# Kernel tuning notes

Hardware: AMD Instinct MI355X
Metric: run time of the kernel (lower is better)

The kernel has to match this reference:

```python
import jax, jax.numpy as jnp
import numpy as np

B, T, D_MODEL, H, D = 2, 2048, 2048, 16, 128


def _rope_tables(t, d_half, base=10000.0):
    inv_freq = 1.0 / (base ** (jnp.arange(d_half, dtype=jnp.float32) / d_half))
    ang = jnp.arange(t, dtype=jnp.float32)[:, None] * inv_freq[None, :]  # (T, D/2)
    return jnp.cos(ang), jnp.sin(ang)


def setup_inputs() -> dict:
    key = jax.random.key(0)
    ks = jax.random.split(key, 5)
    x = jax.random.normal(ks[0], (B, T, D_MODEL), dtype=jnp.float32)
    mask = jnp.tril(jnp.ones((T, T), dtype=bool))  # causal boolean mask
    cos, sin = _rope_tables(T, D // 2)
    std = 1.0 / np.sqrt(D_MODEL)
    Wq = jax.random.normal(ks[1], (D_MODEL, H * D), dtype=jnp.float32) * std
    Wk = jax.random.normal(ks[2], (D_MODEL, H * D), dtype=jnp.float32) * std
    Wv = jax.random.normal(ks[3], (D_MODEL, H * D), dtype=jnp.float32) * std
    Wo = jax.random.normal(ks[4], (H * D, D_MODEL), dtype=jnp.float32) * std
    return {"x": x, "mask": mask, "cos": cos, "sin": sin,
            "Wq": Wq, "Wk": Wk, "Wv": Wv, "Wo": Wo}


def _apply_rope(x, cos, sin):
    # x: (B, H, T, D); cos/sin: (T, D/2)
    half = x.shape[-1] // 2
    x1, x2 = x[..., :half], x[..., half:]
    c = cos[None, None]
    s = sin[None, None]
    return jnp.concatenate([x1 * c - x2 * s, x1 * s + x2 * c], axis=-1)


def reference(x, mask, cos, sin, Wq, Wk, Wv, Wo):
    b, t, _ = x.shape
    scale = 1.0 / np.sqrt(D)
    # projections: (B, T, H*D) -> (B, H, T, D)
    q = (x @ Wq).reshape(b, t, H, D).transpose(0, 2, 1, 3)
    k = (x @ Wk).reshape(b, t, H, D).transpose(0, 2, 1, 3)
    v = (x @ Wv).reshape(b, t, H, D).transpose(0, 2, 1, 3)
    q = _apply_rope(q, cos, sin)
    k = _apply_rope(k, cos, sin)
    scores = jnp.einsum('bhqd,bhkd->bhqk', q, k) * scale
    scores = jnp.where(mask[None, None], scores, jnp.float32(-1e30))
    attn = jax.nn.softmax(scores, axis=-1)
    out = jnp.einsum('bhqk,bhkd->bhqd', attn, v)  # (B, H, T, D)
    out = out.transpose(0, 2, 1, 3).reshape(b, t, H * D)
    return out @ Wo
```

## Files before the change

### kernel.cpp

```cpp
#include <hip/hip_runtime.h>

#define T_SEQ 2048
#define DM    2048
#define NH    16
#define HD    128
#define NROW  4096

typedef __attribute__((ext_vector_type(8))) short short8;
typedef __attribute__((ext_vector_type(4))) float f32x4;
typedef __attribute__((ext_vector_type(16))) float f32x16;

static __device__ __forceinline__ float bf2f(unsigned short h) {
    unsigned int u = ((unsigned int)h) << 16;
    return __builtin_bit_cast(float, u);
}
static __device__ __forceinline__ unsigned short f2bf(float f) {
    unsigned int u = __builtin_bit_cast(unsigned int, f);
    u += 0x7FFFu + ((u >> 16) & 1u);
    return (unsigned short)(u >> 16);
}
static __device__ __forceinline__ unsigned short bf_fast(float f) {
    return (unsigned short)((__builtin_bit_cast(unsigned int, f) + 0x8000u) >> 16);
}

typedef __attribute__((address_space(1))) const unsigned int gas_uint;
typedef __attribute__((address_space(3))) unsigned int las_uint;

static __device__ __forceinline__ void load_lds16(const void* g, void* l) {
    __builtin_amdgcn_global_load_lds((gas_uint*)g, (las_uint*)l, 16, 0, 0);
}

static __device__ __forceinline__ f32x4 mfma_bf16(short8 a, short8 b, f32x4 c) {
    return __builtin_amdgcn_mfma_f32_16x16x32_bf16(a, b, c, 0, 0, 0);
}
static __device__ __forceinline__ f32x16 mfma32_bf16(short8 a, short8 b, f32x16 c) {
    return __builtin_amdgcn_mfma_f32_32x32x16_bf16(a, b, c, 0, 0, 0);
}

__global__ __launch_bounds__(256) void k_cast(const float* __restrict__ x,
                                              unsigned short* __restrict__ xb, int n) {
    int idx = (blockIdx.x * 256 + threadIdx.x) * 4;
    if (idx >= n) return;
    float4 v = *(const float4*)(x + idx);
    ushort4 o;
    o.x = f2bf(v.x); o.y = f2bf(v.y); o.z = f2bf(v.z); o.w = f2bf(v.w);
    *(ushort4*)(xb + idx) = o;
}

__global__ __launch_bounds__(256) void k_transpose(const float* __restrict__ w0, const float* __restrict__ w1,
                                                   const float* __restrict__ w2, const float* __restrict__ w3,
                                                   unsigned short* __restrict__ t0, unsigned short* __restrict__ t1,
                                                   unsigned short* __restrict__ t2, unsigned short* __restrict__ t3) {
    __shared__ float tile[32][33];
    int z = blockIdx.z;
    const float* W = (z == 0) ? w0 : (z == 1) ? w1 : (z == 2) ? w2 : w3;
    unsigned short* Wt = (z == 0) ? t0 : (z == 1) ? t1 : (z == 2) ? t2 : t3;
    int bx = blockIdx.x * 32;
    int by = blockIdx.y * 32;
    int tx = threadIdx.x, ty = threadIdx.y;
#pragma unroll
    for (int i = 0; i < 4; ++i)
        tile[ty + i * 8][tx] = W[(size_t)(by + ty + i * 8) * DM + bx + tx];
    __syncthreads();
#pragma unroll
    for (int i = 0; i < 4; ++i)
        Wt[(size_t)(bx + ty + i * 8) * DM + by + tx] = f2bf(tile[tx][ty + i * 8]);
}

template <bool FOUT>
static __device__ __forceinline__ void gemm_body(const unsigned short* __restrict__ A,
                                                 const unsigned short* __restrict__ Bt,
                                                 unsigned short* __restrict__ Cb,
                                                 float* __restrict__ Cf) {
    __shared__ unsigned short As[128 * 64];
    __shared__ unsigned short Bs[128 * 64];
    const int tid = threadIdx.x;
    const int w = tid >> 6, lane = tid & 63;
    const int col = lane & 15, quad = lane >> 4;
    const int wm = w >> 1, wn = w & 1;
    const size_t m0 = (size_t)blockIdx.y * 128;
    const size_t n0 = (size_t)blockIdx.x * 128;

    f32x4 acc[4][4];
#pragma unroll
    for (int i = 0; i < 4; ++i)
#pragma unroll
        for (int j = 0; j < 4; ++j)
            acc[i][j] = (f32x4){0.f, 0.f, 0.f, 0.f};

    const int lrow = lane >> 3;
    const int gcol = ((lane & 7) ^ lrow) * 8;

    for (int k0 = 0; k0 < DM; k0 += 64) {
#pragma unroll
        for (int c = w; c < 16; c += 4) {
            load_lds16(A + (m0 + c * 8 + lrow) * DM + k0 + gcol, &As[c * 512]);
            load_lds16(Bt + (n0 + c * 8 + lrow) * DM + k0 + gcol, &Bs[c * 512]);
        }
        __syncthreads();
#pragma unroll
        for (int ks = 0; ks < 2; ++ks) {
            short8 af[4], bf[4];
            int g = ks * 4 + quad;
#pragma unroll
            for (int mt = 0; mt < 4; ++mt) {
                int r = wm * 64 + mt * 16 + col;
                af[mt] = *(const short8*)&As[r * 64 + ((g ^ (r & 7)) * 8)];
            }
#pragma unroll
            for (int nt = 0; nt < 4; ++nt) {
                int r = wn * 64 + nt * 16 + col;
                bf[nt] = *(const short8*)&Bs[r * 64 + ((g ^ (r & 7)) * 8)];
            }
#pragma unroll
            for (int mt = 0; mt < 4; ++mt)
#pragma unroll
                for (int nt = 0; nt < 4; ++nt)
                    acc[mt][nt] = mfma_bf16(af[mt], bf[nt], acc[mt][nt]);
        }
        __syncthreads();
    }
#pragma unroll
    for (int mt = 0; mt < 4; ++mt)
#pragma unroll
        for (int nt = 0; nt < 4; ++nt)
#pragma unroll
            for (int reg = 0; reg < 4; ++reg) {
                size_t r = m0 + wm * 64 + mt * 16 + quad * 4 + reg;
                size_t c = n0 + wn * 64 + nt * 16 + col;
                if (FOUT) Cf[r * DM + c] = acc[mt][nt][reg];
                else      Cb[r * DM + c] = f2bf(acc[mt][nt][reg]);
            }
}

__global__ __launch_bounds__(256) void k_gemm_qkv(const unsigned short* __restrict__ xb,
                                                  const unsigned short* __restrict__ wtq,
                                                  const unsigned short* __restrict__ wtk,
                                                  const unsigned short* __restrict__ wtv,
                                                  unsigned short* __restrict__ qb,
                                                  unsigned short* __restrict__ kb,
                                                  unsigned short* __restrict__ vb) {
    int z = blockIdx.z;
    const unsigned short* Bt = (z == 0) ? wtq : (z == 1) ? wtk : wtv;
    unsigned short* C = (z == 0) ? qb : (z == 1) ? kb : vb;
    gemm_body<false>(xb, Bt, C, nullptr);
}

__global__ __launch_bounds__(256) void k_gemm_out(const unsigned short* __restrict__ ob,
                                                  const unsigned short* __restrict__ wto,
                                                  float* __restrict__ out) {
    gemm_body<true>(ob, wto, nullptr, out);
}

__global__ __launch_bounds__(256) void k_rope_k(unsigned short* __restrict__ K,
                                                const float* __restrict__ cosp,
                                                const float* __restrict__ sinp) {
    int idx = blockIdx.x * 256 + threadIdx.x;
    int d4 = (idx & 15) * 4;
    int h = (idx >> 4) & 15;
    int row = idx >> 8;
    int t = row & (T_SEQ - 1);
    size_t base = (size_t)row * DM + h * HD + d4;
    ushort4 x1 = *(const ushort4*)(K + base);
    ushort4 x2 = *(const ushort4*)(K + base + 64);
    float4 c = *(const float4*)(cosp + t * 64 + d4);
    float4 s = *(const float4*)(sinp + t * 64 + d4);
    ushort4 o1, o2;
#pragma unroll
    for (int i = 0; i < 4; ++i) {
        float a1 = bf2f(((const unsigned short*)&x1)[i]);
        float a2 = bf2f(((const unsigned short*)&x2)[i]);
        float cc = ((const float*)&c)[i], ss = ((const float*)&s)[i];
        ((unsigned short*)&o1)[i] = f2bf(a1 * cc - a2 * ss);
        ((unsigned short*)&o2)[i] = f2bf(a1 * ss + a2 * cc);
    }
    *(ushort4*)(K + base) = o1;
    *(ushort4*)(K + base + 64) = o2;
}

__global__ __launch_bounds__(256) void k_vtr(const unsigned short* __restrict__ V,
                                             unsigned short* __restrict__ Vt) {
    __shared__ unsigned short tile[64][68];
    int t0 = blockIdx.x * 64;
    int hd0 = blockIdx.y * 64;
    int b = blockIdx.z;
    int tid = threadIdx.x;
    int rr = tid >> 4, cc = (tid & 15) * 4;
#pragma unroll
    for (int it = 0; it < 4; ++it) {
        int row = it * 16 + rr;
        *(ushort4*)&tile[row][cc] =
            *(const ushort4*)(V + (size_t)(b * T_SEQ + t0 + row) * DM + hd0 + cc);
    }
    __syncthreads();
    int h = hd0 >> 7, d0 = hd0 & 127;
    size_t obase = (size_t)(b * NH + h) * HD;
#pragma unroll
    for (int it = 0; it < 4; ++it) {
        int lhd = it * 16 + rr;
        ushort4 v;
#pragma unroll
        for (int j = 0; j < 4; ++j) ((unsigned short*)&v)[j] = tile[cc + j][lhd];
        *(ushort4*)(Vt + (obase + d0 + lhd) * (size_t)T_SEQ + t0 + cc) = v;
    }
}

#define PST 72
__global__ __launch_bounds__(256) void k_flash(const unsigned short* __restrict__ Q,
                                               const unsigned short* __restrict__ K,
                                               const unsigned short* __restrict__ Vt,
                                               unsigned short* __restrict__ O,
                                               const float* __restrict__ cosp,
                                               const float* __restrict__ sinp) {
    __shared__ unsigned short Ks[64 * 128];
    __shared__ unsigned short Vs[128 * 64];
    __shared__ unsigned short Ps[4][32 * PST];
    const int tid = threadIdx.x;
    const int w = tid >> 6, lane = tid & 63;
    const int col = lane & 31, l5 = lane >> 5;
    const int flat = blockIdx.x | (blockIdx.y << 4) | (blockIdx.z << 8);
    const int j = 15 - (flat >> 5);
    const int hb = flat & 31;
    const int h = hb & 15, b = hb >> 4;
    const int q0 = j * 128;
    const size_t rowbase = ((size_t)b * T_SEQ) * DM + (size_t)h * HD;
    const size_t hbase = ((size_t)b * NH + h) * HD;
    const float SCL = 0.088388347648318447f * 1.4426950408889634f;
    unsigned short* Pw = &Ps[w][0];

    const int t = q0 + w * 32 + col;
    short8 qf[8];
    {
        const unsigned short* qp = Q + rowbase + (size_t)t * DM + l5 * 8;
#pragma unroll
        for (int st = 0; st < 8; ++st)
            qf[st] = *(const short8*)(qp + st * 16);
        const float* cp = cosp + t * 64 + l5 * 8;
        const float* sp = sinp + t * 64 + l5 * 8;
#pragma unroll
        for (int st = 0; st < 4; ++st) {
            float4 c0 = *(const float4*)(cp + st * 16);
            float4 c1 = *(const float4*)(cp + st * 16 + 4);
            float4 s0v = *(const float4*)(sp + st * 16);
            float4 s1v = *(const float4*)(sp + st * 16 + 4);
#pragma unroll
            for (int jj = 0; jj < 8; ++jj) {
                float cv = ((jj < 4) ? ((const float*)&c0)[jj] : ((const float*)&c1)[jj - 4]) * SCL;
                float sv = ((jj < 4) ? ((const float*)&s0v)[jj] : ((const float*)&s1v)[jj - 4]) * SCL;
                float a1 = bf2f((unsigned short)qf[st][jj]);
                float a2 = bf2f((unsigned short)qf[st + 4][jj]);
                qf[st][jj]     = (short)f2bf(a1 * cv - a2 * sv);
                qf[st + 4][jj] = (short)f2bf(a1 * sv + a2 * cv);
            }
        }
    }

    f32x16 o[4];
#pragma unroll
    for (int i = 0; i < 4; ++i) o[i] = (f32x16)(0.f);
    float m_i = -1e30f, l_i = 0.f;

    const int kt_max = 2 * j + 1;
    const int kt_lim = (q0 + w * 32 + 31) >> 6;
    const int cswz = col & 7;

    for (int kt = 0; kt <= kt_max; ++kt) {
        const int k0 = kt * 64;
        __syncthreads();
#pragma unroll
        for (int c = 0; c < 4; ++c) {
            const int c4 = w * 4 + c;
            const int krow = c4 * 4 + (lane >> 4);
            const int kpos = lane & 15;
            load_lds16(K + rowbase + (size_t)(k0 + krow) * DM + ((kpos ^ (krow & 7)) * 8),
                       &Ks[c4 * 512]);
            const int vrow = c4 * 8 + (lane >> 3);
            const int vpos = lane & 7;
            load_lds16(Vt + (hbase + vrow) * (size_t)T_SEQ + k0 + ((vpos ^ (vrow & 7)) * 8),
                       &Vs[c4 * 512]);
        }
        __syncthreads();
        if (kt > kt_lim) continue;

        f32x16 s0 = (f32x16)(0.f), s1 = (f32x16)(0.f);
#pragma unroll
        for (int st = 0; st < 8; ++st) {
            const int dg = (2 * st + l5) ^ cswz;
            short8 kf0 = *(const short8*)&Ks[col * 128 + dg * 8];
            short8 kf1 = *(const short8*)&Ks[col * 128 + 4096 + dg * 8];
            s0 = mfma32_bf16(kf0, qf[st], s0);
            s1 = mfma32_bf16(kf1, qf[st], s1);
        }

        if (k0 + 63 > q0 + w * 32) {
            const int kb = k0 + 4 * l5;
#pragma unroll
            for (int r = 0; r < 16; ++r) {
                const int key = kb + (r & 3) + 8 * (r >> 2);
                if (key > t) s0[r] = -1e30f;
                if (key + 32 > t) s1[r] = -1e30f;
            }
        }

        float mx = -1e30f;
#pragma unroll
        for (int r = 0; r < 16; ++r) mx = fmaxf(mx, fmaxf(s0[r], s1[r]));
        mx = fmaxf(mx, __shfl_xor(mx, 32));
        const float mnew = fmaxf(m_i, mx);
        const float alpha = __builtin_amdgcn_exp2f(m_i - mnew);
        m_i = mnew;
        float sum = 0.f;
#pragma unroll
        for (int r = 0; r < 16; ++r) {
            float p0 = __builtin_amdgcn_exp2f(s0[r] - mnew);
            float p1 = __builtin_amdgcn_exp2f(s1[r] - mnew);
            s0[r] = p0; s1[r] = p1;
            sum += p0 + p1;
        }
        sum += __shfl_xor(sum, 32);
        l_i = l_i * alpha + sum;
#pragma unroll
        for (int i = 0; i < 4; ++i) o[i] *= alpha;

#pragma unroll
        for (int g = 0; g < 4; ++g) {
            ushort4 a4, b4;
#pragma unroll
            for (int i = 0; i < 4; ++i) {
                ((unsigned short*)&a4)[i] = bf_fast(s0[g * 4 + i]);
                ((unsigned short*)&b4)[i] = bf_fast(s1[g * 4 + i]);
            }
            *(ushort4*)(Pw + col * PST + g * 8 + 4 * l5)      = a4;
            *(ushort4*)(Pw + col * PST + 32 + g * 8 + 4 * l5) = b4;
        }
        short8 pb[4];
#pragma unroll
        for (int st = 0; st < 4; ++st)
            pb[st] = *(const short8*)(Pw + col * PST + st * 16 + l5 * 8);

#pragma unroll
        for (int ms = 0; ms < 4; ++ms) {
            const int drow = (ms * 32 + col) * 64;
#pragma unroll
            for (int st = 0; st < 4; ++st) {
                const int kg = (2 * st + l5) ^ cswz;
                short8 vf = *(const short8*)&Vs[drow + kg * 8];
                o[ms] = mfma32_bf16(vf, pb[st], o[ms]);
            }
        }
    }

    const float inv = __builtin_amdgcn_rcpf(l_i);
    unsigned short* op = O + rowbase + (size_t)t * DM;
#pragma unroll
    for (int ms = 0; ms < 4; ++ms)
#pragma unroll
        for (int g = 0; g < 4; ++g) {
            ushort4 st4;
#pragma unroll
            for (int i = 0; i < 4; ++i)
                ((unsigned short*)&st4)[i] = bf_fast(o[ms][g * 4 + i] * inv);
            *(ushort4*)(op + ms * 32 + g * 8 + 4 * l5) = st4;
        }
}

extern "C" void kernel_launch(void* const* d_in, const int* in_sizes, int n_in,
                              void* d_out, int out_size, void* d_ws, size_t ws_size,
                              hipStream_t stream) {
    const float* x    = (const float*)d_in[0];
    const float* cosp = (const float*)d_in[2];
    const float* sinp = (const float*)d_in[3];
    const float* Wq   = (const float*)d_in[4];
    const float* Wk   = (const float*)d_in[5];
    const float* Wv   = (const float*)d_in[6];
    const float* Wo   = (const float*)d_in[7];
    float* out = (float*)d_out;

    unsigned short* xb  = (unsigned short*)d_ws;
    unsigned short* wtq = xb  + (size_t)NROW * DM;
    unsigned short* wtk = wtq + (size_t)DM * DM;
    unsigned short* wtv = wtk + (size_t)DM * DM;
    unsigned short* wto = wtv + (size_t)DM * DM;
    unsigned short* qb  = wto + (size_t)DM * DM;
    unsigned short* kb  = qb  + (size_t)NROW * DM;
    unsigned short* vb  = kb  + (size_t)NROW * DM;
    unsigned short* ob  = vb  + (size_t)NROW * DM;
    unsigned short* vt  = xb;

    hipLaunchKernelGGL(k_cast, dim3(8192), dim3(256), 0, stream, x, xb, NROW * DM);
    hipLaunchKernelGGL(k_transpose, dim3(64, 64, 4), dim3(32, 8), 0, stream,
                       Wq, Wk, Wv, Wo, wtq, wtk, wtv, wto);
    hipLaunchKernelGGL(k_gemm_qkv, dim3(16, 32, 3), dim3(256), 0, stream,
                       xb, wtq, wtk, wtv, qb, kb, vb);
    hipLaunchKernelGGL(k_rope_k, dim3(4096), dim3(256), 0, stream, kb, cosp, sinp);
    hipLaunchKernelGGL(k_vtr, dim3(32, 32, 2), dim3(256), 0, stream, vb, vt);
    hipLaunchKernelGGL(k_flash, dim3(16, 16, 2), dim3(256), 0, stream,
                       qb, kb, vt, ob, cosp, sinp);
    hipLaunchKernelGGL(k_gemm_out, dim3(16, 32, 1), dim3(256), 0, stream, ob, wto, out);
}
```

Baseline: 392.2 us.

## Restructure flash attention into single-wave blocks handling two query sub-tiles

New measurement: 637.8 us. +62.6%, slower.

```diff
diff --git a/kernel.cpp b/kernel.cpp
--- a/kernel.cpp
+++ b/kernel.cpp
@@ -206,31 +206,31 @@
 }
 
 #define PST 72
-__global__ __launch_bounds__(256) void k_flash(const unsigned short* __restrict__ Q,
-                                               const unsigned short* __restrict__ K,
-                                               const unsigned short* __restrict__ Vt,
-                                               unsigned short* __restrict__ O,
-                                               const float* __restrict__ cosp,
-                                               const float* __restrict__ sinp) {
-    __shared__ unsigned short Ks[64 * 128];
-    __shared__ unsigned short Vs[128 * 64];
-    __shared__ unsigned short Ps[4][32 * PST];
-    const int tid = threadIdx.x;
-    const int w = tid >> 6, lane = tid & 63;
+__global__ __launch_bounds__(64, 2) void k_flash(const unsigned short* __restrict__ Q,
+                                                 const unsigned short* __restrict__ K,
+                                                 const unsigned short* __restrict__ Vt,
+                                                 unsigned short* __restrict__ O,
+                                                 const float* __restrict__ cosp,
+                                                 const float* __restrict__ sinp) {
+    __shared__ unsigned short Ks[32 * 128];
+    __shared__ unsigned short Vs[128 * 32];
+    __shared__ unsigned short Ps[64 * PST];
+    const int lane = threadIdx.x;
     const int col = lane & 31, l5 = lane >> 5;
-    const int flat = blockIdx.x | (blockIdx.y << 4) | (blockIdx.z << 8);
-    const int j = 15 - (flat >> 5);
-    const int hb = flat & 31;
-    const int h = hb & 15, b = hb >> 4;
-    const int q0 = j * 128;
+    const int flat = blockIdx.x;
+    const int j = 31 - (flat >> 5);
+    const int bh = flat & 31;
+    const int h = bh & 15, b = bh >> 4;
+    const int q0 = j * 64;
     const size_t rowbase = ((size_t)b * T_SEQ) * DM + (size_t)h * HD;
     const size_t hbase = ((size_t)b * NH + h) * HD;
     const float SCL = 0.088388347648318447f * 1.4426950408889634f;
-    unsigned short* Pw = &Ps[w][0];
-
-    const int t = q0 + w * 32 + col;
-    short8 qf[8];
-    {
+
+    const int tA = q0 + col;
+    const int tB = q0 + 32 + col;
+
+    short8 qfA[8], qfB[8];
+    auto load_q = [&](int t, short8* qf) {
         const unsigned short* qp = Q + rowbase + (size_t)t * DM + l5 * 8;
 #pragma unroll
         for (int st = 0; st < 8; ++st)
@@ -253,115 +253,119 @@
                 qf[st + 4][jj] = (short)f2bf(a1 * sv + a2 * cv);
             }
         }
+    };
+    load_q(tA, qfA);
+    load_q(tB, qfB);
+
+    f32x16 oA[4], oB[4];
+#pragma unroll
+    for (int i = 0; i < 4; ++i) { oA[i] = (f32x16)(0.f); oB[i] = (f32x16)(0.f); }
+    float mA = -1e30f, lA = 0.f, mB = -1e30f, lB = 0.f;
+
+    const int cs7 = col & 7;
+    const int kt_lim = 2 * j + 1;
+
+    for (int kt = 0; kt <= kt_lim; ++kt) {
+        const int k0 = kt * 32;
+        const bool bothQ = (kt <= 2 * j);
+
+#pragma unroll
+        for (int c = 0; c < 8; ++c) {
+            const int s = c * 64 + lane;
+            const int key = s >> 4, ck = s & 15;
+            load_lds16(K + rowbase + (size_t)(k0 + key) * DM + ((ck ^ (key & 7)) * 8),
+                       &Ks[c * 512]);
+            const int d = s >> 2, kg = s & 3;
+            load_lds16(Vt + (hbase + d) * (size_t)T_SEQ + k0 + ((kg ^ ((d >> 1) & 3)) * 8),
+                       &Vs[c * 512]);
+        }
+        __builtin_amdgcn_s_waitcnt(0);
+
+        f32x16 sA = (f32x16)(0.f), sB = (f32x16)(0.f);
+#pragma unroll
+        for (int st = 0; st < 8; ++st) {
+            short8 kf = *(const short8*)&Ks[col * 128 + (((st * 2 + l5) ^ cs7) * 8)];
+            sB = mfma32_bf16(kf, qfB[st], sB);
+            if (bothQ) sA = mfma32_bf16(kf, qfA[st], sA);
+        }
+
+        if (kt == 2 * j) {
+#pragma unroll
+            for (int r = 0; r < 16; ++r) {
+                const int key = k0 + (r & 3) + 8 * (r >> 2) + 4 * l5;
+                if (key > tA) sA[r] = -1e30f;
+            }
+        } else if (kt == 2 * j + 1) {
+#pragma unroll
+            for (int r = 0; r < 16; ++r) {
+                const int key = k0 + (r & 3) + 8 * (r >> 2) + 4 * l5;
+                if (key > tB) sB[r] = -1e30f;
+            }
+        }
+
+        auto softmax_half = [&](f32x16& s, f32x16* o, float& m_i, float& l_i, int prow) {
+            float mx = -1e30f;
+#pragma unroll
+            for (int r = 0; r < 16; ++r) mx = fmaxf(mx, s[r]);
+            mx = fmaxf(mx, __shfl_xor(mx, 32));
+            const float mnew = fmaxf(m_i, mx);
+            const float alpha = __builtin_amdgcn_exp2f(m_i - mnew);
+            m_i = mnew;
+            float sum = 0.f;
+#pragma unroll
+            for (int g = 0; g < 4; ++g) {
+                ushort4 st4;
+#pragma unroll
+                for (int i = 0; i < 4; ++i) {
+                    float p = __builtin_amdgcn_exp2f(s[g * 4 + i] - mnew);
+                    sum += p;
+                    ((unsigned short*)&st4)[i] = bf_fast(p);
+                }
+                *(ushort4*)(Ps + prow * PST + 4 * l5 + 8 * g) = st4;
+            }
+            sum += __shfl_xor(sum, 32);
+            l_i = l_i * alpha + sum;
+#pragma unroll
+            for (int i = 0; i < 4; ++i) o[i] *= alpha;
+        };
+        softmax_half(sB, oB, mB, lB, 32 + col);
+        if (bothQ) softmax_half(sA, oA, mA, lA, col);
+
+        short8 pbA[2], pbB[2];
+#pragma unroll
+        for (int st = 0; st < 2; ++st) {
+            pbB[st] = *(const short8*)&Ps[(32 + col) * PST + st * 16 + l5 * 8];
+            if (bothQ) pbA[st] = *(const short8*)&Ps[col * PST + st * 16 + l5 * 8];
+        }
+#pragma unroll
+        for (int ms = 0; ms < 4; ++ms) {
+            const int d = ms * 32 + col;
+            const int dswz = (d >> 1) & 3;
+#pragma unroll
+            for (int st = 0; st < 2; ++st) {
+                short8 vf = *(const short8*)&Vs[d * 32 + (((st * 2 + l5) ^ dswz) * 8)];
+                oB[ms] = mfma32_bf16(vf, pbB[st], oB[ms]);
+                if (bothQ) oA[ms] = mfma32_bf16(vf, pbA[st], oA[ms]);
+            }
+        }
     }
 
-    f32x16 o[4];
-#pragma unroll
-    for (int i = 0; i < 4; ++i) o[i] = (f32x16)(0.f);
-    float m_i = -1e30f, l_i = 0.f;
-
-    const int kt_max = 2 * j + 1;
-    const int kt_lim = (q0 + w * 32 + 31) >> 6;
-    const int cswz = col & 7;
-
-    for (int kt = 0; kt <= kt_max; ++kt) {
-        const int k0 = kt * 64;
-        __syncthreads();
-#pragma unroll
-        for (int c = 0; c < 4; ++c) {
-            const int c4 = w * 4 + c;
-            const int krow = c4 * 4 + (lane >> 4);
-            const int kpos = lane & 15;
-            load_lds16(K + rowbase + (size_t)(k0 + krow) * DM + ((kpos ^ (krow & 7)) * 8),
-                       &Ks[c4 * 512]);
-            const int vrow = c4 * 8 + (lane >> 3);
-            const int vpos = lane & 7;
-            load_lds16(Vt + (hbase + vrow) * (size_t)T_SEQ + k0 + ((vpos ^ (vrow & 7)) * 8),
-                       &Vs[c4 * 512]);
-        }
-        __syncthreads();
-        if (kt > kt_lim) continue;
-
-        f32x16 s0 = (f32x16)(0.f), s1 = (f32x16)(0.f);
-#pragma unroll
-        for (int st = 0; st < 8; ++st) {
-            const int dg = (2 * st + l5) ^ cswz;
-            short8 kf0 = *(const short8*)&Ks[col * 128 + dg * 8];
-            short8 kf1 = *(const short8*)&Ks[col * 128 + 4096 + dg * 8];
-            s0 = mfma32_bf16(kf0, qf[st], s0);
-            s1 = mfma32_bf16(kf1, qf[st], s1);
-        }
-
-        if (k0 + 63 > q0 + w * 32) {
-            const int kb = k0 + 4 * l5;
-#pragma unroll
-            for (int r = 0; r < 16; ++r) {
-                const int key = kb + (r & 3) + 8 * (r >> 2);
-                if (key > t) s0[r] = -1e30f;
-                if (key + 32 > t) s1[r] = -1e30f;
-            }
-        }
-
-        float mx = -1e30f;
-#pragma unroll
-        for (int r = 0; r < 16; ++r) mx = fmaxf(mx, fmaxf(s0[r], s1[r]));
-        mx = fmaxf(mx, __shfl_xor(mx, 32));
-        const float mnew = fmaxf(m_i, mx);
-        const float alpha = __builtin_amdgcn_exp2f(m_i - mnew);
-        m_i = mnew;
-        float sum = 0.f;
-#pragma unroll
-        for (int r = 0; r < 16; ++r) {
-            float p0 = __builtin_amdgcn_exp2f(s0[r] - mnew);
-            float p1 = __builtin_amdgcn_exp2f(s1[r] - mnew);
-            s0[r] = p0; s1[r] = p1;
-            sum += p0 + p1;
-        }
-        sum += __shfl_xor(sum, 32);
-        l_i = l_i * alpha + sum;
-#pragma unroll
-        for (int i = 0; i < 4; ++i) o[i] *= alpha;
-
-#pragma unroll
-        for (int g = 0; g < 4; ++g) {
-            ushort4 a4, b4;
-#pragma unroll
-            for (int i = 0; i < 4; ++i) {
-                ((unsigned short*)&a4)[i] = bf_fast(s0[g * 4 + i]);
-                ((unsigned short*)&b4)[i] = bf_fast(s1[g * 4 + i]);
-            }
-            *(ushort4*)(Pw + col * PST + g * 8 + 4 * l5)      = a4;
-            *(ushort4*)(Pw + col * PST + 32 + g * 8 + 4 * l5) = b4;
-        }
-        short8 pb[4];
-#pragma unroll
-        for (int st = 0; st < 4; ++st)
-            pb[st] = *(const short8*)(Pw + col * PST + st * 16 + l5 * 8);
-
-#pragma unroll
-        for (int ms = 0; ms < 4; ++ms) {
-            const int drow = (ms * 32 + col) * 64;
-#pragma unroll
-            for (int st = 0; st < 4; ++st) {
-                const int kg = (2 * st + l5) ^ cswz;
-                short8 vf = *(const short8*)&Vs[drow + kg * 8];
-                o[ms] = mfma32_bf16(vf, pb[st], o[ms]);
-            }
-        }
-    }
-
-    const float inv = __builtin_amdgcn_rcpf(l_i);
-    unsigned short* op = O + rowbase + (size_t)t * DM;
-#pragma unroll
-    for (int ms = 0; ms < 4; ++ms)
-#pragma unroll
-        for (int g = 0; g < 4; ++g) {
-            ushort4 st4;
-#pragma unroll
-            for (int i = 0; i < 4; ++i)
-                ((unsigned short*)&st4)[i] = bf_fast(o[ms][g * 4 + i] * inv);
-            *(ushort4*)(op + ms * 32 + g * 8 + 4 * l5) = st4;
-        }
+    auto finish = [&](const f32x16* o, float l_i, int t) {
+        const float inv = __builtin_amdgcn_rcpf(l_i);
+        unsigned short* op = O + rowbase + (size_t)t * DM;
+#pragma unroll
+        for (int ms = 0; ms < 4; ++ms)
+#pragma unroll
+            for (int g = 0; g < 4; ++g) {
+                ushort4 st4;
+#pragma unroll
+                for (int i = 0; i < 4; ++i)
+                    ((unsigned short*)&st4)[i] = bf_fast(o[ms][g * 4 + i] * inv);
+                *(ushort4*)(op + ms * 32 + 8 * g + 4 * l5) = st4;
+            }
+    };
+    finish(oA, lA, tA);
+    finish(oB, lB, tB);
 }
 
 extern "C" void kernel_launch(void* const* d_in, const int* in_sizes, int n_in,
@@ -394,7 +398,7 @@
                        xb, wtq, wtk, wtv, qb, kb, vb);
     hipLaunchKernelGGL(k_rope_k, dim3(4096), dim3(256), 0, stream, kb, cosp, sinp);
     hipLaunchKernelGGL(k_vtr, dim3(32, 32, 2), dim3(256), 0, stream, vb, vt);
-    hipLaunchKernelGGL(k_flash, dim3(16, 16, 2), dim3(256), 0, stream,
+    hipLaunchKernelGGL(k_flash, dim3(1024), dim3(64), 0, stream,
                        qb, kb, vt, ob, cosp, sinp);
     hipLaunchKernelGGL(k_gemm_out, dim3(16, 32, 1), dim3(256), 0, stream, ob, wto, out);
 }
```

## Write V transposed from QKV GEMM epilogue and merge cast/transpose prep kernels

Applied to the files above, without the earlier changes.

Measured after the change: 399.9 us. No clear change (+2.0%).

```diff
diff --git a/kernel.cpp b/kernel.cpp
--- a/kernel.cpp
+++ b/kernel.cpp
@@ -37,27 +37,29 @@
     return __builtin_amdgcn_mfma_f32_32x32x16_bf16(a, b, c, 0, 0, 0);
 }
 
-__global__ __launch_bounds__(256) void k_cast(const float* __restrict__ x,
-                                              unsigned short* __restrict__ xb, int n) {
-    int idx = (blockIdx.x * 256 + threadIdx.x) * 4;
-    if (idx >= n) return;
-    float4 v = *(const float4*)(x + idx);
-    ushort4 o;
-    o.x = f2bf(v.x); o.y = f2bf(v.y); o.z = f2bf(v.z); o.w = f2bf(v.w);
-    *(ushort4*)(xb + idx) = o;
-}
-
-__global__ __launch_bounds__(256) void k_transpose(const float* __restrict__ w0, const float* __restrict__ w1,
-                                                   const float* __restrict__ w2, const float* __restrict__ w3,
-                                                   unsigned short* __restrict__ t0, unsigned short* __restrict__ t1,
-                                                   unsigned short* __restrict__ t2, unsigned short* __restrict__ t3) {
+__global__ __launch_bounds__(256) void k_prep(const float* __restrict__ x,
+                                              unsigned short* __restrict__ xb,
+                                              const float* __restrict__ w0, const float* __restrict__ w1,
+                                              const float* __restrict__ w2, const float* __restrict__ w3,
+                                              unsigned short* __restrict__ t0, unsigned short* __restrict__ t1,
+                                              unsigned short* __restrict__ t2, unsigned short* __restrict__ t3) {
     __shared__ float tile[32][33];
-    int z = blockIdx.z;
+    int f = blockIdx.x;
+    if (f < 8192) {
+        int idx = (f * 256 + threadIdx.x) * 4;
+        float4 v = *(const float4*)(x + idx);
+        ushort4 o;
+        o.x = f2bf(v.x); o.y = f2bf(v.y); o.z = f2bf(v.z); o.w = f2bf(v.w);
+        *(ushort4*)(xb + idx) = o;
+        return;
+    }
+    f -= 8192;
+    int z = f >> 12;
     const float* W = (z == 0) ? w0 : (z == 1) ? w1 : (z == 2) ? w2 : w3;
     unsigned short* Wt = (z == 0) ? t0 : (z == 1) ? t1 : (z == 2) ? t2 : t3;
-    int bx = blockIdx.x * 32;
-    int by = blockIdx.y * 32;
-    int tx = threadIdx.x, ty = threadIdx.y;
+    int bx = (f & 63) * 32;
+    int by = ((f >> 6) & 63) * 32;
+    int tx = threadIdx.x & 31, ty = threadIdx.x >> 5;
 #pragma unroll
     for (int i = 0; i < 4; ++i)
         tile[ty + i * 8][tx] = W[(size_t)(by + ty + i * 8) * DM + bx + tx];
@@ -67,7 +69,7 @@
         Wt[(size_t)(bx + ty + i * 8) * DM + by + tx] = f2bf(tile[tx][ty + i * 8]);
 }
 
-template <bool FOUT>
+template <int MODE>
 static __device__ __forceinline__ void gemm_body(const unsigned short* __restrict__ A,
                                                  const unsigned short* __restrict__ Bt,
                                                  unsigned short* __restrict__ Cb,
@@ -120,6 +122,24 @@
         }
         __syncthreads();
     }
+    if (MODE == 2) {
+#pragma unroll
+        for (int mt = 0; mt < 4; ++mt) {
+            const int r0 = (int)m0 + wm * 64 + mt * 16 + quad * 4;
+            const int b_ = r0 >> 11, t_ = r0 & (T_SEQ - 1);
+#pragma unroll
+            for (int nt = 0; nt < 4; ++nt) {
+                const int c = (int)n0 + wn * 64 + nt * 16 + col;
+                size_t addr = ((size_t)(b_ * NH + (c >> 7)) * HD + (c & 127)) * (size_t)T_SEQ + t_;
+                ushort4 st;
+#pragma unroll
+                for (int reg = 0; reg < 4; ++reg)
+                    ((unsigned short*)&st)[reg] = f2bf(acc[mt][nt][reg]);
+                *(ushort4*)(Cb + addr) = st;
+            }
+        }
+        return;
+    }
 #pragma unroll
     for (int mt = 0; mt < 4; ++mt)
 #pragma unroll
@@ -128,8 +148,8 @@
             for (int reg = 0; reg < 4; ++reg) {
                 size_t r = m0 + wm * 64 + mt * 16 + quad * 4 + reg;
                 size_t c = n0 + wn * 64 + nt * 16 + col;
-                if (FOUT) Cf[r * DM + c] = acc[mt][nt][reg];
-                else      Cb[r * DM + c] = f2bf(acc[mt][nt][reg]);
+                if (MODE == 1) Cf[r * DM + c] = acc[mt][nt][reg];
+                else           Cb[r * DM + c] = f2bf(acc[mt][nt][reg]);
             }
 }
 
@@ -139,17 +159,21 @@
                                                   const unsigned short* __restrict__ wtv,
                                                   unsigned short* __restrict__ qb,
                                                   unsigned short* __restrict__ kb,
-                                                  unsigned short* __restrict__ vb) {
+                                                  unsigned short* __restrict__ vt) {
     int z = blockIdx.z;
-    const unsigned short* Bt = (z == 0) ? wtq : (z == 1) ? wtk : wtv;
-    unsigned short* C = (z == 0) ? qb : (z == 1) ? kb : vb;
-    gemm_body<false>(xb, Bt, C, nullptr);
+    if (z == 2) {
+        gemm_body<2>(xb, wtv, vt, nullptr);
+    } else {
+        const unsigned short* Bt = (z == 0) ? wtq : wtk;
+        unsigned short* C = (z == 0) ? qb : kb;
+        gemm_body<0>(xb, Bt, C, nullptr);
+    }
 }
 
 __global__ __launch_bounds__(256) void k_gemm_out(const unsigned short* __restrict__ ob,
                                                   const unsigned short* __restrict__ wto,
                                                   float* __restrict__ out) {
-    gemm_body<true>(ob, wto, nullptr, out);
+    gemm_body<1>(ob, wto, nullptr, out);
 }
 
 __global__ __launch_bounds__(256) void k_rope_k(unsigned short* __restrict__ K,
@@ -176,33 +200,6 @@
     }
     *(ushort4*)(K + base) = o1;
     *(ushort4*)(K + base + 64) = o2;
-}
-
-__global__ __launch_bounds__(256) void k_vtr(const unsigned short* __restrict__ V,
-                                             unsigned short* __restrict__ Vt) {
-    __shared__ unsigned short tile[64][68];
-    int t0 = blockIdx.x * 64;
-    int hd0 = blockIdx.y * 64;
-    int b = blockIdx.z;
-    int tid = threadIdx.x;
-    int rr = tid >> 4, cc = (tid & 15) * 4;
-#pragma unroll
-    for (int it = 0; it < 4; ++it) {
-        int row = it * 16 + rr;
-        *(ushort4*)&tile[row][cc] =
-            *(const ushort4*)(V + (size_t)(b * T_SEQ + t0 + row) * DM + hd0 + cc);
-    }
-    __syncthreads();
-    int h = hd0 >> 7, d0 = hd0 & 127;
-    size_t obase = (size_t)(b * NH + h) * HD;
-#pragma unroll
-    for (int it = 0; it < 4; ++it) {
-        int lhd = it * 16 + rr;
-        ushort4 v;
-#pragma unroll
-        for (int j = 0; j < 4; ++j) ((unsigned short*)&v)[j] = tile[cc + j][lhd];
-        *(ushort4*)(Vt + (obase + d0 + lhd) * (size_t)T_SEQ + t0 + cc) = v;
-    }
 }
 
 #define PST 72
@@ -383,17 +380,14 @@
     unsigned short* wto = wtv + (size_t)DM * DM;
     unsigned short* qb  = wto + (size_t)DM * DM;
     unsigned short* kb  = qb  + (size_t)NROW * DM;
-    unsigned short* vb  = kb  + (size_t)NROW * DM;
-    unsigned short* ob  = vb  + (size_t)NROW * DM;
-    unsigned short* vt  = xb;
-
-    hipLaunchKernelGGL(k_cast, dim3(8192), dim3(256), 0, stream, x, xb, NROW * DM);
-    hipLaunchKernelGGL(k_transpose, dim3(64, 64, 4), dim3(32, 8), 0, stream,
-                       Wq, Wk, Wv, Wo, wtq, wtk, wtv, wto);
+    unsigned short* vt  = kb  + (size_t)NROW * DM;
+    unsigned short* ob  = vt  + (size_t)NROW * DM;
+
+    hipLaunchKernelGGL(k_prep, dim3(8192 + 16384), dim3(256), 0, stream,
+                       x, xb, Wq, Wk, Wv, Wo, wtq, wtk, wtv, wto);
     hipLaunchKernelGGL(k_gemm_qkv, dim3(16, 32, 3), dim3(256), 0, stream,
-                       xb, wtq, wtk, wtv, qb, kb, vb);
+                       xb, wtq, wtk, wtv, qb, kb, vt);
     hipLaunchKernelGGL(k_rope_k, dim3(4096), dim3(256), 0, stream, kb, cosp, sinp);
-    hipLaunchKernelGGL(k_vtr, dim3(32, 32, 2), dim3(256), 0, stream, vb, vt);
     hipLaunchKernelGGL(k_flash, dim3(16, 16, 2), dim3(256), 0, stream,
                        qb, kb, vt, ob, cosp, sinp);
     hipLaunchKernelGGL(k_gemm_out, dim3(16, 32, 1), dim3(256), 0, stream, ob, wto, out);
```
